# Performance work log

Measured on AMD Instinct MI355X. Metric: run time of the kernel, lower is better.

Reference implementation:

```python
import jax, jax.numpy as jnp
import numpy as np

B, L, H, D_IN = 64, 4096, 128, 3

def setup_inputs() -> dict:
    key = jax.random.key(0)
    ks = jax.random.split(key, 9)
    def lin_w(k, fan_in, shape):
        bound = 1.0 / np.sqrt(fan_in)
        return jax.random.uniform(k, shape, jnp.float32, -bound, bound)
    return {
        "x": jax.random.normal(ks[0], (B, L, D_IN), jnp.float32),
        "Wp": lin_w(ks[1], D_IN, (D_IN, H)), "bp": lin_w(ks[2], D_IN, (H,)),
        "Wz": lin_w(ks[3], H, (H, H)),      "bz": lin_w(ks[4], H, (H,)),
        "Wh": lin_w(ks[5], H, (H, H)),      "bh": lin_w(ks[6], H, (H,)),
        "Wg": lin_w(ks[7], H, (H, 1)),      "bg": lin_w(ks[8], H, (1,)),
    }

def reference(x, Wp, bp, Wz, bz, Wh, bh, Wg, bg):
    # Batched projections across all timesteps (B, L, H)
    inp = x @ Wp + bp                      # input_proj
    z = jax.nn.sigmoid(inp @ Wz + bz)      # update gate
    h_tilde = jnp.tanh(inp @ Wh + bh)      # candidate
    # Linear recurrence h_t = a_t * h_{t-1} + b_t, h_{-1} = 0
    a = 1.0 - z
    b = z * h_tilde
    def combine(c1, c2):
        a1, b1 = c1
        a2, b2 = c2
        return (a1 * a2, b1 * a2 + b2)
    _, h = jax.lax.associative_scan(combine, (a, b), axis=1)  # h_t (since h_{-1}=0)
    # Readout uses h BEFORE the update at each step: preds_t = gauss_head(h_{t-1})
    h_prev = jnp.concatenate([jnp.zeros_like(h[:, :1]), h[:, :-1]], axis=1)
    preds = h_prev @ Wg + bg               # (B, L, 1)
    return preds
```

## Files before the change

### kernel.cpp

```cpp
#include <hip/hip_runtime.h>
#include <hip/hip_bf16.h>
#include <stdint.h>

#define B_   64
#define L_   4096
#define H_   128
#define T_   64
#define C_   (L_/T_)
#define BH_  (B_*H_)
#define PADI 136

typedef __attribute__((ext_vector_type(8))) short short8;
typedef __attribute__((ext_vector_type(4))) short short4v;
typedef __attribute__((ext_vector_type(4))) float floatx4;

#define LOG2E 1.44269504088896340736f

__device__ __forceinline__ unsigned short f2bf(float f){
    unsigned int u = __float_as_uint(f);
    u += 0x7FFFu + ((u >> 16) & 1u);
    return (unsigned short)(u >> 16);
}
__device__ __forceinline__ float bf2f(unsigned short s){
    return __uint_as_float(((unsigned int)s) << 16);
}

__global__ void prep_w(const float* __restrict__ Wz, const float* __restrict__ Wh,
                       unsigned short* __restrict__ WzT, unsigned short* __restrict__ WhT){
    int b = blockIdx.x;
    const float* W = (b < 16) ? Wz : Wh;
    unsigned short* WT = (b < 16) ? WzT : WhT;
    int b16 = b & 15, tid = threadIdx.x;
    #pragma unroll
    for (int it = 0; it < 4; ++it){
        int idx = b16*1024 + it*256 + tid;
        int n = idx >> 7, k = idx & 127;
        WT[idx] = f2bf(W[k*H_ + n]);
    }
}


__global__ __launch_bounds__(256, 4)
void gates_agg(const float* __restrict__ x,
               const float* __restrict__ Wp, const float* __restrict__ bp,
               const float* __restrict__ bz, const float* __restrict__ bh,
               const float* __restrict__ Wg,
               const unsigned short* __restrict__ WzT,
               const unsigned short* __restrict__ WhT,
               float* __restrict__ aggA, float* __restrict__ aggH,
               float* __restrict__ sloc, unsigned short* __restrict__ pw_g)
{
    __shared__ __align__(16) unsigned short s_ab[H_*H_];
    __shared__ float s_bz[H_], s_bh[H_], s_wg[H_];
    __shared__ float s_part[256];
    unsigned short* inp_lds = s_ab;

    const int bid = blockIdx.x;
    const int bb  = bid / C_;
    const int cc  = bid % C_;
    const int t0g = cc * T_;
    const int tid = threadIdx.x;
    const int wv = tid >> 6, lane = tid & 63, quad = lane >> 4, l15 = lane & 15;

    if (tid < H_){ s_bz[tid] = bz[tid]; s_bh[tid] = bh[tid]; s_wg[tid] = Wg[tid]; }

    #pragma unroll
    for (int it = 0; it < 4; ++it){
        int idx = tid + it*256;
        int t = idx >> 4, h0 = (idx & 15) * 8;
        const float* xr = x + ((size_t)bb*L_ + t0g + t)*3;
        float x0 = xr[0], x1 = xr[1], x2 = xr[2];
        short8 pk;
        #pragma unroll
        for (int m = 0; m < 8; ++m){
            int hh = h0 + m;
            float v = bp[hh];
            v = fmaf(x0, Wp[hh],      v);
            v = fmaf(x1, Wp[H_+hh],   v);
            v = fmaf(x2, Wp[2*H_+hh], v);
            pk[m] = (short)f2bf(v);
        }
        *(short8*)&inp_lds[t*PADI + h0] = pk;
    }
    __syncthreads();

    const int ct0 = wv*2;

    floatx4 accz[4][2];
    #pragma unroll
    for (int r = 0; r < 4; ++r)
        #pragma unroll
        for (int c = 0; c < 2; ++c) accz[r][c] = (floatx4){0.f,0.f,0.f,0.f};
    #pragma unroll
    for (int kk = 0; kk < 4; ++kk){
        short8 af[4], bfr[2];
        #pragma unroll
        for (int r = 0; r < 4; ++r)
            af[r] = *(const short8*)&inp_lds[(r*16 + l15)*PADI + kk*32 + quad*8];
        #pragma unroll
        for (int c = 0; c < 2; ++c)
            bfr[c] = *(const short8*)&WzT[((ct0+c)*16 + l15)*H_ + kk*32 + quad*8];
        #pragma unroll
        for (int r = 0; r < 4; ++r)
            #pragma unroll
            for (int c = 0; c < 2; ++c)
                accz[r][c] = __builtin_amdgcn_mfma_f32_16x16x32_bf16(af[r], bfr[c], accz[r][c], 0, 0, 0);
    }

    floatx4 acch[4][2];
    #pragma unroll
    for (int r = 0; r < 4; ++r)
        #pragma unroll
        for (int c = 0; c < 2; ++c) acch[r][c] = (floatx4){0.f,0.f,0.f,0.f};
    #pragma unroll
    for (int kk = 0; kk < 4; ++kk){
        short8 af[4], bfr[2];
        #pragma unroll
        for (int r = 0; r < 4; ++r)
            af[r] = *(const short8*)&inp_lds[(r*16 + l15)*PADI + kk*32 + quad*8];
        #pragma unroll
        for (int c = 0; c < 2; ++c)
            bfr[c] = *(const short8*)&WhT[((ct0+c)*16 + l15)*H_ + kk*32 + quad*8];
        #pragma unroll
        for (int r = 0; r < 4; ++r)
            #pragma unroll
            for (int c = 0; c < 2; ++c)
                acch[r][c] = __builtin_amdgcn_mfma_f32_16x16x32_bf16(af[r], bfr[c], acch[r][c], 0, 0, 0);
    }
    __syncthreads();

    #pragma unroll
    for (int r = 0; r < 4; ++r){
        #pragma unroll
        for (int c = 0; c < 2; ++c){
            int col = (ct0+c)*16 + l15;
            float vbz = s_bz[col], vbh = s_bh[col];
            short8 pk;
            #pragma unroll
            for (int e = 0; e < 4; ++e){
                float szb = accz[r][c][e] + vbz;
                float a = __builtin_amdgcn_rcpf(1.0f + __builtin_amdgcn_exp2f(szb * LOG2E));
                unsigned short abf = f2bf(a);
                float af_ = bf2f(abf);
                float z = 1.0f - af_;
                float shb = acch[r][c][e] + vbh;
                float e2 = __builtin_amdgcn_exp2f(2.0f*LOG2E*fabsf(shb));
                float tt = 1.0f - 2.0f*__builtin_amdgcn_rcpf(e2 + 1.0f);
                float bt = z * copysignf(tt, shb);
                pk[2*e]   = (short)abf;
                pk[2*e+1] = (short)f2bf(bt);
            }
            int ch = (r*4 + quad) ^ l15;
            *(short8*)&s_ab[col*H_ + ch*8] = pk;
        }
    }
    __syncthreads();

    if (tid < H_){
        float A = 1.0f, h = 0.0f;
        float wgv = s_wg[tid];
        unsigned short* pwdst = pw_g + (size_t)bid*(T_*H_) + tid*T_;
        #pragma unroll
        for (int t4 = 0; t4 < 16; ++t4){
            int base = tid*H_ + ((t4 ^ (tid & 15)) << 3);
            short8 pr = *(const short8*)&s_ab[base];
            short8 wb;
            short4v pq;
            #pragma unroll
            for (int e = 0; e < 4; ++e){
                float aa = bf2f((unsigned short)pr[2*e]);
                float bv = bf2f((unsigned short)pr[2*e+1]);
                unsigned short hwq = f2bf(h * wgv);
                unsigned short pwq = f2bf(A * wgv);
                wb[2*e]   = (short)hwq;
                wb[2*e+1] = (short)pwq;
                pq[e]     = (short)pwq;
                A *= aa;
                h = fmaf(aa, h, bv);
            }
            *(short8*)&s_ab[base] = wb;
            *(short4v*)&pwdst[t4*4] = pq;
        }
        aggA[cc*BH_ + bb*H_ + tid] = A;
        aggH[cc*BH_ + bb*H_ + tid] = h;
    }
    __syncthreads();

    {
        int t = tid & 63, w4 = tid >> 6;
        int t4 = t >> 2, e2 = (t & 3)*2;
        float s = 0.0f;
        #pragma unroll
        for (int j = 0; j < 32; ++j){
            int col = w4*32 + j;
            s += bf2f(s_ab[col*H_ + ((t4 ^ (col & 15)) << 3) + e2]);
        }
        s_part[w4*64 + t] = s;
    }
    __syncthreads();
    if (tid < 64)
        sloc[(size_t)bid*T_ + tid] =
            s_part[tid] + s_part[64+tid] + s_part[128+tid] + s_part[192+tid];
}

__global__ __launch_bounds__(256, 4)
void apply2(const unsigned short* __restrict__ pw_g,
            const float* __restrict__ aggA, const float* __restrict__ aggH,
            const float* __restrict__ sloc, const float* __restrict__ bg,
            float* __restrict__ preds)
{
    __shared__ __align__(16) unsigned short s_pw[T_*H_];
    __shared__ float s_c[H_];
    __shared__ float s_part[256];
    const int bid = blockIdx.x;
    const int bb  = bid / C_;
    const int cc  = bid % C_;
    const int t0g = cc * T_;
    const int tid = threadIdx.x;
    const int wv = tid >> 6, lane = tid & 63;

    {
        const char* src = (const char*)(pw_g + (size_t)bid*(T_*H_));
        char* dst = (char*)s_pw;
        #pragma unroll
        for (int i = 0; i < 4; ++i){
            int off = (wv*4 + i)*1024;
            __builtin_amdgcn_global_load_lds(
                (const __attribute__((address_space(1))) unsigned int*)(src + off + lane*16),
                (__attribute__((address_space(3))) unsigned int*)(dst + off), 16, 0, 0);
        }
    }
    if (tid < H_){
        float cval = 0.0f;
        #pragma unroll
        for (int ch = 0; ch < C_; ++ch){
            float ga = aggA[ch*BH_ + bb*H_ + tid];
            float gh = aggH[ch*BH_ + bb*H_ + tid];
            bool in = ch < cc;
            cval = fmaf(in ? ga : 1.0f, cval, in ? gh : 0.0f);
        }
        s_c[tid] = cval;
    }
    __syncthreads();

    {
        int t = tid & 63, w4 = tid >> 6;
        float s = 0.0f;
        #pragma unroll
        for (int j = 0; j < 32; ++j){
            int col = w4*32 + j;
            s += s_c[col] * bf2f(s_pw[col*T_ + t]);
        }
        s_part[w4*64 + t] = s;
    }
    __syncthreads();
    if (tid < 64){
        float s = s_part[tid] + s_part[64+tid] + s_part[128+tid] + s_part[192+tid];
        preds[(size_t)bb*L_ + t0g + tid] = s + sloc[(size_t)bid*T_ + tid] + bg[0];
    }
}

extern "C" void kernel_launch(void* const* d_in, const int* in_sizes, int n_in,
                              void* d_out, int out_size, void* d_ws, size_t ws_size,
                              hipStream_t stream){
    const float* x  = (const float*)d_in[0];
    const float* Wp = (const float*)d_in[1];
    const float* bp = (const float*)d_in[2];
    const float* Wz = (const float*)d_in[3];
    const float* bz = (const float*)d_in[4];
    const float* Wh = (const float*)d_in[5];
    const float* bh = (const float*)d_in[6];
    const float* Wg = (const float*)d_in[7];
    const float* bg = (const float*)d_in[8];
    float* preds = (float*)d_out;

    uint8_t* w8 = (uint8_t*)d_ws;
    unsigned short* WzT = (unsigned short*)(w8);
    unsigned short* WhT = (unsigned short*)(w8 + 32768);
    float* aggA = (float*)(w8 + 65536);
    float* aggH = (float*)(w8 + 65536 + 4u*BH_*C_);
    float* sloc = (float*)(w8 + 65536 + 8u*BH_*C_);
    unsigned short* pw_g = (unsigned short*)(w8 + 65536 + 12u*BH_*C_);

    hipLaunchKernelGGL(prep_w, dim3(32), dim3(256), 0, stream, Wz, Wh, WzT, WhT);
    hipLaunchKernelGGL(gates_agg, dim3(B_*C_), dim3(256), 0, stream,
                       x, Wp, bp, bz, bh, Wg, WzT, WhT, aggA, aggH, sloc, pw_g);
    hipLaunchKernelGGL(apply2, dim3(B_*C_), dim3(256), 0, stream,
                       pw_g, aggA, aggH, sloc, bg, preds);
}
```

Measured before the change: 160.9 us.

## Hoist projection weights, coalesce pw writeback, read pw directly from global in apply

The input projection now loads the Wp and bp columns into registers once per thread instead of once per timestep iteration. In the scan phase, the pw stores go to LDS only, and a separate cooperative pass then copies them to global memory as coalesced writes spread over all 256 threads, replacing the strided per-thread stores from the 128 scan threads. The apply kernel drops its LDS staging of pw and reads it directly from global memory in the dot-product loop. This saves LDS and a sync-dependent async copy, at the risk of less efficient global reads in apply.

New measurement: 159.9 us. No clear change (-0.6%).

```diff
diff --git a/kernel.cpp b/kernel.cpp
--- a/kernel.cpp
+++ b/kernel.cpp
@@ -64,23 +64,30 @@
 
     if (tid < H_){ s_bz[tid] = bz[tid]; s_bh[tid] = bh[tid]; s_wg[tid] = Wg[tid]; }
 
-    #pragma unroll
-    for (int it = 0; it < 4; ++it){
-        int idx = tid + it*256;
-        int t = idx >> 4, h0 = (idx & 15) * 8;
-        const float* xr = x + ((size_t)bb*L_ + t0g + t)*3;
-        float x0 = xr[0], x1 = xr[1], x2 = xr[2];
-        short8 pk;
+    {
+        const int h0 = (tid & 15) * 8;
+        float w0[8], w1[8], w2[8], b0[8];
         #pragma unroll
         for (int m = 0; m < 8; ++m){
-            int hh = h0 + m;
-            float v = bp[hh];
-            v = fmaf(x0, Wp[hh],      v);
-            v = fmaf(x1, Wp[H_+hh],   v);
-            v = fmaf(x2, Wp[2*H_+hh], v);
-            pk[m] = (short)f2bf(v);
-        }
-        *(short8*)&inp_lds[t*PADI + h0] = pk;
+            w0[m] = Wp[h0+m]; w1[m] = Wp[H_+h0+m]; w2[m] = Wp[2*H_+h0+m];
+            b0[m] = bp[h0+m];
+        }
+        #pragma unroll
+        for (int it = 0; it < 4; ++it){
+            int t = (tid >> 4) + it*16;
+            const float* xr = x + ((size_t)bb*L_ + t0g + t)*3;
+            float x0 = xr[0], x1 = xr[1], x2 = xr[2];
+            short8 pk;
+            #pragma unroll
+            for (int m = 0; m < 8; ++m){
+                float v = b0[m];
+                v = fmaf(x0, w0[m], v);
+                v = fmaf(x1, w1[m], v);
+                v = fmaf(x2, w2[m], v);
+                pk[m] = (short)f2bf(v);
+            }
+            *(short8*)&inp_lds[t*PADI + h0] = pk;
+        }
     }
     __syncthreads();
 
@@ -159,32 +166,39 @@
     if (tid < H_){
         float A = 1.0f, h = 0.0f;
         float wgv = s_wg[tid];
-        unsigned short* pwdst = pw_g + (size_t)bid*(T_*H_) + tid*T_;
         #pragma unroll
         for (int t4 = 0; t4 < 16; ++t4){
             int base = tid*H_ + ((t4 ^ (tid & 15)) << 3);
             short8 pr = *(const short8*)&s_ab[base];
             short8 wb;
-            short4v pq;
             #pragma unroll
             for (int e = 0; e < 4; ++e){
                 float aa = bf2f((unsigned short)pr[2*e]);
                 float bv = bf2f((unsigned short)pr[2*e+1]);
-                unsigned short hwq = f2bf(h * wgv);
-                unsigned short pwq = f2bf(A * wgv);
-                wb[2*e]   = (short)hwq;
-                wb[2*e+1] = (short)pwq;
-                pq[e]     = (short)pwq;
+                wb[2*e]   = (short)f2bf(h * wgv);
+                wb[2*e+1] = (short)f2bf(A * wgv);
                 A *= aa;
                 h = fmaf(aa, h, bv);
             }
             *(short8*)&s_ab[base] = wb;
-            *(short4v*)&pwdst[t4*4] = pq;
         }
         aggA[cc*BH_ + bb*H_ + tid] = A;
         aggH[cc*BH_ + bb*H_ + tid] = h;
     }
     __syncthreads();
+
+    {
+        unsigned short* dst = pw_g + (size_t)bid*(T_*H_);
+        #pragma unroll
+        for (int i = 0; i < 8; ++i){
+            int idx = i*256 + tid;
+            int col = idx >> 4, t4 = idx & 15;
+            short8 pr = *(const short8*)&s_ab[col*H_ + ((t4 ^ (col & 15)) << 3)];
+            short4v pw4;
+            pw4[0] = pr[1]; pw4[1] = pr[3]; pw4[2] = pr[5]; pw4[3] = pr[7];
+            *(short4v*)&dst[col*T_ + t4*4] = pw4;
+        }
+    }
 
     {
         int t = tid & 63, w4 = tid >> 6;
@@ -209,7 +223,6 @@
             const float* __restrict__ sloc, const float* __restrict__ bg,
             float* __restrict__ preds)
 {
-    __shared__ __align__(16) unsigned short s_pw[T_*H_];
     __shared__ float s_c[H_];
     __shared__ float s_part[256];
     const int bid = blockIdx.x;
@@ -217,19 +230,7 @@
     const int cc  = bid % C_;
     const int t0g = cc * T_;
     const int tid = threadIdx.x;
-    const int wv = tid >> 6, lane = tid & 63;
-
-    {
-        const char* src = (const char*)(pw_g + (size_t)bid*(T_*H_));
-        char* dst = (char*)s_pw;
-        #pragma unroll
-        for (int i = 0; i < 4; ++i){
-            int off = (wv*4 + i)*1024;
-            __builtin_amdgcn_global_load_lds(
-                (const __attribute__((address_space(1))) unsigned int*)(src + off + lane*16),
-                (__attribute__((address_space(3))) unsigned int*)(dst + off), 16, 0, 0);
-        }
-    }
+
     if (tid < H_){
         float cval = 0.0f;
         #pragma unroll
@@ -244,12 +245,13 @@
     __syncthreads();
 
     {
+        const unsigned short* src = pw_g + (size_t)bid*(T_*H_);
         int t = tid & 63, w4 = tid >> 6;
         float s = 0.0f;
         #pragma unroll
         for (int j = 0; j < 32; ++j){
             int col = w4*32 + j;
-            s += s_c[col] * bf2f(s_pw[col*T_ + t]);
+            s += s_c[col] * bf2f(src[col*T_ + t]);
         }
         s_part[w4*64 + t] = s;
     }
```
